# Kernel tuning notes

Hardware: AMD Instinct MI355X
Metric: run time of the kernel (lower is better)

## Reference

```python
import jax, jax.numpy as jnp
import numpy as np

B, C, H, W = 64, 256, 64, 64
HEADS = 8
Q = 16
FH = 512
EPS = 1e-6


def setup_inputs() -> dict:
    key = jax.random.key(0)
    ks = jax.random.split(key, 4)
    def init(k, shape, fan_in):
        return jax.random.normal(k, shape, jnp.float32) * (1.0 / np.sqrt(fan_in))
    return {
        "x": jax.random.normal(ks[0], (B, C, H, W), jnp.float32),
        "ln_gamma": jnp.ones((C,), jnp.float32),
        "ln_beta": jnp.zeros((C,), jnp.float32),
        # grouped 1x1 conv weight: torch shape [Q*h, C/h, 1, 1] -> [h, Q, C/h]
        "attn_w": init(ks[1], (HEADS, Q, C // HEADS), C // HEADS),
        "val_w": init(ks[2], (C, C), C),
        "val_b": jnp.zeros((C,), jnp.float32),
        "fin_w": init(ks[3], (FH, C * Q), C * Q),
        "fin_b": jnp.zeros((FH,), jnp.float32),
    }


def reference(x, ln_gamma, ln_beta, attn_w, val_w, val_b, fin_w, fin_b):
    B_, C_, H_, W_ = x.shape
    L = H_ * W_
    xf = x.reshape(B_, C_, L)  # [B, C, HW]
    # LayerNorm2d: normalize over channel dim (permute in torch == axis=1 here)
    mu = jnp.mean(xf, axis=1, keepdims=True)
    var = jnp.mean((xf - mu) ** 2, axis=1, keepdims=True)
    xn = (xf - mu) * jax.lax.rsqrt(var + EPS) * ln_gamma[:, None] + ln_beta[:, None]
    # grouped 1x1 conv: each head sees its own C/h channel slice
    xh = xn.reshape(B_, HEADS, C_ // HEADS, L)
    logits = jnp.einsum('hqc,bhcl->bhql', attn_w, xh)  # [B, h, Q, HW]
    Aw = jax.nn.softmax(logits, axis=-1)
    # value projection: full 1x1 conv with bias
    V = jnp.einsum('ec,bcl->bel', val_w, xn) + val_b[None, :, None]  # [B, C, HW]
    Vh = V.reshape(B_, HEADS, C_ // HEADS, L)
    # weighted pooling (bmm): [B, h, Q, d]
    A = jnp.einsum('bhql,bhdl->bhqd', Aw, Vh)
    Aflat = A.reshape(B_, Q * C_)  # matches torch reshape order (h, q, d)
    return Aflat @ fin_w.T + fin_b
```

## Files before the change

### kernel.cpp

```cpp
#include <hip/hip_runtime.h>

typedef unsigned short u16;
typedef unsigned int u32;

#define B_   64
#define C_   256
#define L_   4096
#define NH   8
#define NQ   16
#define DH   32
#define HQ   128
#define FHN  512
#define EPS_ 1e-6f

#define WS_WC    0
#define WS_SWG   8192
#define WS_CB    8704
#define WS_VGC   9216
#define WS_WG1   140288
#define WS_WB1   141312
#define WS_DENP  142336
#define WS_SNUP  404480
#define WS_A     666624
#define WS_APART 1715200

typedef __attribute__((ext_vector_type(8))) short bf16x8;
typedef __attribute__((ext_vector_type(4))) float f32x4;

__device__ __forceinline__ u16 f32_to_bf16(float f) {
    u32 u = __float_as_uint(f);
    u32 r = u + 0x7fffu + ((u >> 16) & 1u);
    return (u16)(r >> 16);
}
__device__ __forceinline__ float bf16_to_f32(u16 h) {
    return __uint_as_float(((u32)h) << 16);
}
__device__ __forceinline__ u32 pk2(u16 lo, u16 hi) {
    return (u32)lo | ((u32)hi << 16);
}

__global__ __launch_bounds__(256) void k_prep(
    const float* __restrict__ attn_w, const float* __restrict__ gamma,
    const float* __restrict__ beta, u16* __restrict__ wc,
    float* __restrict__ Swg, float* __restrict__ Cb)
{
    int t = threadIdx.x;
    if (t >= HQ) return;
    int h = t >> 4;
    float sw = 0.f, cb = 0.f;
    for (int c = 0; c < DH; c++) {
        float w = attn_w[t * DH + c];
        u16 hb = f32_to_bf16(w * gamma[h * DH + c]);
        wc[t * DH + c] = hb;
        sw += bf16_to_f32(hb);
        cb += w * beta[h * DH + c];
    }
    Swg[t] = sw;
    Cb[t] = cb;
}

__global__ __launch_bounds__(256) void k_prepv(
    const float* __restrict__ val_w, const float* __restrict__ gamma,
    const float* __restrict__ beta, u16* __restrict__ VGc,
    float* __restrict__ Wg1, float* __restrict__ Wb1)
{
    int t = threadIdx.x;
    int e = blockIdx.x * 4 + (t >> 6);
    int lane = t & 63;
    float4 w  = *(const float4*)(val_w + (size_t)e * C_ + lane * 4);
    float4 g  = *(const float4*)(gamma + lane * 4);
    float4 bt = *(const float4*)(beta + lane * 4);
    u16 h0 = f32_to_bf16(w.x * g.x);
    u16 h1 = f32_to_bf16(w.y * g.y);
    u16 h2 = f32_to_bf16(w.z * g.z);
    u16 h3 = f32_to_bf16(w.w * g.w);
    uint2 pk;
    pk.x = pk2(h0, h1);
    pk.y = pk2(h2, h3);
    *(uint2*)(VGc + (size_t)e * C_ + lane * 4) = pk;
    float sg = bf16_to_f32(h0) + bf16_to_f32(h1) + bf16_to_f32(h2) + bf16_to_f32(h3);
    float sb = w.x * bt.x + w.y * bt.y + w.z * bt.z + w.w * bt.w;
    #pragma unroll
    for (int off = 1; off < 64; off <<= 1) {
        sg += __shfl_xor(sg, off);
        sb += __shfl_xor(sb, off);
    }
    if (lane == 0) { Wg1[e] = sg; Wb1[e] = sb; }
}

__global__ __launch_bounds__(256) void k_fused(
    const float* __restrict__ x, const u16* __restrict__ wc,
    const float* __restrict__ Swg, const float* __restrict__ Cb,
    const u16* __restrict__ VGc, float* __restrict__ Apart,
    float* __restrict__ DenP, float* __restrict__ SnuP)
{
    __shared__ __align__(16) char POOL[67584];
    u16* const XT  = (u16*)POOL;
    u16* const EA  = (u16*)(POOL + 16896);
    u16* const XCb = (u16*)(POOL + 27136);
    __shared__ float smu[32], srs[32];
    int t = threadIdx.x;
    int lane = t & 63, wv = t >> 6;
    int lane15 = lane & 15, quad = lane >> 4;
    int ks = blockIdx.x, b = blockIdx.y;
    int lbase = ks * 512;
    int m0 = (wv & 1) * 64, n0 = (wv >> 1) * 128;

    bf16x8 af[2];
    float swr[2][4], cbr[2][4];
    #pragma unroll
    for (int s = 0; s < 2; s++) {
        int h = wv * 2 + s;
        af[s] = *(const bf16x8*)(wc + (size_t)(h * 16 + lane15) * DH + quad * 8);
        #pragma unroll
        for (int r = 0; r < 4; r++) {
            int hq = h * 16 + quad * 4 + r;
            swr[s][r] = Swg[hq];
            cbr[s][r] = Cb[hq];
        }
    }

    const float* xR = x + ((size_t)b * C_ + t) * L_ + lbase;

    float4 fr[8];
    uint4 pr[4];
    auto loadregs = [&](int k) {
        int o = k * 32;
        #pragma unroll
        for (int i = 0; i < 8; i++) fr[i] = *(const float4*)(xR + o + i * 4);
    };
    auto cvtregs = [&]() {
        const float* pf = (const float*)fr;
        u16 hh[32];
        #pragma unroll
        for (int e = 0; e < 32; e++) hh[e] = f32_to_bf16(pf[e]);
        #pragma unroll
        for (int i = 0; i < 4; i++) {
            uint4 w;
            w.x = pk2(hh[i * 8 + 0], hh[i * 8 + 1]);
            w.y = pk2(hh[i * 8 + 2], hh[i * 8 + 3]);
            w.z = pk2(hh[i * 8 + 4], hh[i * 8 + 5]);
            w.w = pk2(hh[i * 8 + 6], hh[i * 8 + 7]);
            pr[i] = w;
        }
    };
    auto write_xc = [&](int buf) {
        #pragma unroll
        for (int i = 0; i < 4; i++)
            *(uint4*)&XCb[buf * 8192 + t * 32 + ((i ^ (t & 3)) * 8)] = pr[i];
    };
    auto write_xt = [&]() {
        const u16* ph = (const u16*)pr;
        #pragma unroll
        for (int e = 0; e < 32; e++) XT[e * 264 + t] = ph[e];
    };

    f32x4 acc[4][8];
    #pragma unroll
    for (int i = 0; i < 4; i++)
        #pragma unroll
        for (int j = 0; j < 8; j++) {
            f32x4 z = {0.f, 0.f, 0.f, 0.f};
            acc[i][j] = z;
        }
    float se[2][4] = {}, sm[2][4] = {};

    int l_loc = t >> 3, g = t & 7;

    loadregs(0);
    cvtregs();
    write_xt();
    write_xc(0);
    loadregs(1);
    __syncthreads();

    for (int k = 0; k < 16; k++) {
        int cur = k & 1;

        {
            const u16* row = XT + l_loc * 264 + g * 32;
            float s = 0.f, q = 0.f;
            #pragma unroll
            for (int j = 0; j < 4; j++) {
                uint4 v = *(const uint4*)(row + j * 8);
                u32 ww[4] = {v.x, v.y, v.z, v.w};
                #pragma unroll
                for (int e = 0; e < 4; e++) {
                    float f0 = __uint_as_float(ww[e] << 16);
                    float f1 = __uint_as_float(ww[e] & 0xffff0000u);
                    s += f0 + f1;
                    q += f0 * f0 + f1 * f1;
                }
            }
            #pragma unroll
            for (int off = 1; off < 8; off <<= 1) {
                s += __shfl_xor(s, off);
                q += __shfl_xor(q, off);
            }
            if (g == 0) {
                float mm = s * (1.f / C_);
                float vv = fmaxf(q * (1.f / C_) - mm * mm, 0.f) + EPS_;
                smu[l_loc] = mm;
                srs[l_loc] = rsqrtf(vv);
            }
        }
        __syncthreads();

        #pragma unroll
        for (int half = 0; half < 2; half++) {
            float m_l = smu[half * 16 + lane15];
            float r_l = srs[half * 16 + lane15];
            #pragma unroll
            for (int s = 0; s < 2; s++) {
                int h = wv * 2 + s;
                bf16x8 bfrag = *(const bf16x8*)(XT + (half * 16 + lane15) * 264 + h * DH + quad * 8);
                f32x4 z = {0.f, 0.f, 0.f, 0.f};
                f32x4 c4 = __builtin_amdgcn_mfma_f32_16x16x32_bf16(af[s], bfrag, z, 0, 0, 0);
                #pragma unroll
                for (int r = 0; r < 4; r++) {
                    float logit = r_l * (c4[r] - m_l * swr[s][r]) + cbr[s][r];
                    float e = __expf(logit);
                    float ers = e * r_l;
                    EA[(h * 16 + quad * 4 + r) * 40 + half * 16 + lane15] = f32_to_bf16(ers);
                    se[s][r] += e;
                    sm[s][r] += ers * m_l;
                }
            }
        }
        __syncthreads();

        if (k < 15) { cvtregs(); write_xt(); write_xc(cur ^ 1); }
        if (k < 14) loadregs(k + 2);

        bf16x8 a[4];
        #pragma unroll
        for (int i = 0; i < 4; i++)
            a[i] = *(const bf16x8*)&EA[(m0 + i * 16 + lane15) * 40 + quad * 8];
        #pragma unroll
        for (int j = 0; j < 8; j++) {
            int row = n0 + j * 16 + lane15;
            bf16x8 bbj = *(const bf16x8*)&XCb[cur * 8192 + row * 32 + ((quad ^ (row & 3)) * 8)];
            #pragma unroll
            for (int i = 0; i < 4; i++)
                acc[i][j] = __builtin_amdgcn_mfma_f32_16x16x32_bf16(a[i], bbj, acc[i][j], 0, 0, 0);
        }
        __syncthreads();
    }

    u16* const P = (u16*)POOL;
    #pragma unroll
    for (int i = 0; i < 4; i++)
        #pragma unroll
        for (int j = 0; j < 8; j++) {
            int row = m0 + i * 16 + quad * 4;
            int col = n0 + j * 16 + lane15;
            #pragma unroll
            for (int r = 0; r < 4; r++)
                P[(row + r) * 264 + col] = f32_to_bf16(acc[i][j][r]);
        }
    __syncthreads();

    float* ApB = Apart + (((size_t)ks * B_ + b) * HQ) * DH;
    #pragma unroll
    for (int s = 0; s < 2; s++) {
        int h = wv * 2 + s;
        #pragma unroll
        for (int dt = 0; dt < 2; dt++) {
            f32x4 c2 = {0.f, 0.f, 0.f, 0.f};
            #pragma unroll
            for (int kk = 0; kk < 8; kk++) {
                bf16x8 a = *(const bf16x8*)&P[(h * 16 + lane15) * 264 + kk * 32 + quad * 8];
                bf16x8 vg = *(const bf16x8*)(VGc + (size_t)(h * DH + dt * 16 + lane15) * C_ + kk * 32 + quad * 8);
                c2 = __builtin_amdgcn_mfma_f32_16x16x32_bf16(a, vg, c2, 0, 0, 0);
            }
            #pragma unroll
            for (int r = 0; r < 4; r++)
                ApB[(size_t)(h * 16 + quad * 4 + r) * DH + dt * 16 + lane15] = c2[r];
        }
    }

    #pragma unroll
    for (int s = 0; s < 2; s++)
        #pragma unroll
        for (int r = 0; r < 4; r++) {
            float v = se[s][r], w = sm[s][r];
            #pragma unroll
            for (int off = 1; off < 16; off <<= 1) {
                v += __shfl_xor(v, off);
                w += __shfl_xor(w, off);
            }
            if (lane15 == 0) {
                int row = b * HQ + (wv * 2 + s) * 16 + quad * 4 + r;
                DenP[ks * (B_ * HQ) + row] = v;
                SnuP[ks * (B_ * HQ) + row] = w;
            }
        }
}

__global__ __launch_bounds__(256) void k_reduce(
    const float* __restrict__ Apart, const float* __restrict__ DenP,
    const float* __restrict__ SnuP, const float* __restrict__ Wg1,
    const float* __restrict__ Wb1, const float* __restrict__ val_b,
    float* __restrict__ A)
{
    __shared__ float sden[32], ssnu[32];
    int t = threadIdx.x;
    int q4 = blockIdx.x, b = blockIdx.y;
    int hq0 = q4 * 32;
    if (t < 32) {
        int row = b * HQ + hq0 + t;
        float d = 0.f, sn = 0.f;
        #pragma unroll
        for (int s = 0; s < 8; s++) {
            d  += DenP[s * (B_ * HQ) + row];
            sn += SnuP[s * (B_ * HQ) + row];
        }
        sden[t] = d;
        ssnu[t] = sn;
    }
    __syncthreads();
    #pragma unroll
    for (int i = 0; i < 4; i++) {
        int idx = i * 256 + t;
        int r32 = idx >> 5, d = idx & 31;
        int hq = hq0 + r32;
        float v = 0.f;
        #pragma unroll
        for (int s = 0; s < 8; s++)
            v += Apart[(((size_t)s * B_ + b) * HQ + hq) * DH + d];
        int hd = (hq >> 4) * DH + d;
        A[((size_t)b * HQ + hq) * DH + d] =
            (v - ssnu[r32] * Wg1[hd]) / sden[r32] + Wb1[hd] + val_b[hd];
    }
}

__global__ __launch_bounds__(256) void k_final(
    const float* __restrict__ A, const float* __restrict__ fin_w,
    const float* __restrict__ fin_b, float* __restrict__ out)
{
    __shared__ float At[64 * 129];
    __shared__ float Fw[32 * 129];
    int t = threadIdx.x;
    int kc = blockIdx.x, ft = blockIdx.y;
    int k0 = kc * 128;

    #pragma unroll
    for (int w = 0; w < 8; w++) {
        int s = t + w * 256;
        int row = s >> 5, seg = s & 31;
        float4 v = *(const float4*)(A + (size_t)row * 4096 + k0 + seg * 4);
        const float* pf = (const float*)&v;
        #pragma unroll
        for (int e = 0; e < 4; e++) At[row * 129 + seg * 4 + e] = pf[e];
    }
    #pragma unroll
    for (int w = 0; w < 4; w++) {
        int s = t + w * 256;
        int row = s >> 5, seg = s & 31;
        float4 v = *(const float4*)(fin_w + (size_t)(ft * 32 + row) * 4096 + k0 + seg * 4);
        const float* pf = (const float*)&v;
        #pragma unroll
        for (int e = 0; e < 4; e++) Fw[row * 129 + seg * 4 + e] = pf[e];
    }
    __syncthreads();

    int tb = t >> 3, tf = t & 7;
    float acc[2][4];
    #pragma unroll
    for (int e = 0; e < 2; e++)
        #pragma unroll
        for (int j = 0; j < 4; j++) acc[e][j] = 0.f;

    for (int k = 0; k < 128; k++) {
        float a0 = At[(tb * 2) * 129 + k];
        float a1 = At[(tb * 2 + 1) * 129 + k];
        #pragma unroll
        for (int j = 0; j < 4; j++) {
            float f = Fw[(tf * 4 + j) * 129 + k];
            acc[0][j] += a0 * f;
            acc[1][j] += a1 * f;
        }
    }
    #pragma unroll
    for (int e = 0; e < 2; e++) {
        int brow = tb * 2 + e;
        #pragma unroll
        for (int j = 0; j < 4; j++) {
            int f = ft * 32 + tf * 4 + j;
            float v = acc[e][j];
            if (kc == 0) v += fin_b[f];
            atomicAdd(&out[(size_t)brow * FHN + f], v);
        }
    }
}

extern "C" void kernel_launch(void* const* d_in, const int* in_sizes, int n_in,
                              void* d_out, int out_size, void* d_ws, size_t ws_size,
                              hipStream_t stream) {
    const float* x      = (const float*)d_in[0];
    const float* gamma  = (const float*)d_in[1];
    const float* beta   = (const float*)d_in[2];
    const float* attn_w = (const float*)d_in[3];
    const float* val_w  = (const float*)d_in[4];
    const float* val_b  = (const float*)d_in[5];
    const float* fin_w  = (const float*)d_in[6];
    const float* fin_b  = (const float*)d_in[7];
    float* out = (float*)d_out;
    char* ws = (char*)d_ws;

    u16*   wc    = (u16*)(ws + WS_WC);
    float* Swg   = (float*)(ws + WS_SWG);
    float* Cb    = (float*)(ws + WS_CB);
    u16*   VGc   = (u16*)(ws + WS_VGC);
    float* Wg1   = (float*)(ws + WS_WG1);
    float* Wb1   = (float*)(ws + WS_WB1);
    float* DenP  = (float*)(ws + WS_DENP);
    float* SnuP  = (float*)(ws + WS_SNUP);
    float* A     = (float*)(ws + WS_A);
    float* Apart = (float*)(ws + WS_APART);

    hipMemsetAsync(out, 0, (size_t)B_ * FHN * sizeof(float), stream);

    k_prep<<<dim3(1), dim3(256), 0, stream>>>(attn_w, gamma, beta, wc, Swg, Cb);
    k_prepv<<<dim3(64), dim3(256), 0, stream>>>(val_w, gamma, beta, VGc, Wg1, Wb1);
    k_fused<<<dim3(8, 64), dim3(256), 0, stream>>>(x, wc, Swg, Cb, VGc, Apart,
                                                   DenP, SnuP);
    k_reduce<<<dim3(4, 64), dim3(256), 0, stream>>>(Apart, DenP, SnuP, Wg1, Wb1,
                                                    val_b, A);
    k_final<<<dim3(32, 16), dim3(256), 0, stream>>>(A, fin_w, fin_b, out);
}
```

Measured before the change: 431.0 us.

## Double block to 512 threads, single-buffer XC, shrink per-wave tiles

Result: slower. 582.1 us (+35.1%).

```diff
diff --git a/kernel.cpp b/kernel.cpp
--- a/kernel.cpp
+++ b/kernel.cpp
@@ -88,100 +88,96 @@
     if (lane == 0) { Wg1[e] = sg; Wb1[e] = sb; }
 }
 
-__global__ __launch_bounds__(256) void k_fused(
+__global__ __launch_bounds__(512, 4) void k_fused(
     const float* __restrict__ x, const u16* __restrict__ wc,
     const float* __restrict__ Swg, const float* __restrict__ Cb,
     const u16* __restrict__ VGc, float* __restrict__ Apart,
     float* __restrict__ DenP, float* __restrict__ SnuP)
 {
-    __shared__ __align__(16) char POOL[67584];
-    u16* const XT  = (u16*)POOL;
-    u16* const EA  = (u16*)(POOL + 16896);
-    u16* const XCb = (u16*)(POOL + 27136);
+    __shared__ __align__(16) char POOL[42496];
+    u16* const XT = (u16*)POOL;
+    u16* const EA = (u16*)(POOL + 16896);
+    u16* const XC = (u16*)(POOL + 26112);
     __shared__ float smu[32], srs[32];
     int t = threadIdx.x;
     int lane = t & 63, wv = t >> 6;
     int lane15 = lane & 15, quad = lane >> 4;
     int ks = blockIdx.x, b = blockIdx.y;
     int lbase = ks * 512;
-    int m0 = (wv & 1) * 64, n0 = (wv >> 1) * 128;
-
-    bf16x8 af[2];
-    float swr[2][4], cbr[2][4];
-    #pragma unroll
-    for (int s = 0; s < 2; s++) {
-        int h = wv * 2 + s;
-        af[s] = *(const bf16x8*)(wc + (size_t)(h * 16 + lane15) * DH + quad * 8);
-        #pragma unroll
-        for (int r = 0; r < 4; r++) {
-            int hq = h * 16 + quad * 4 + r;
-            swr[s][r] = Swg[hq];
-            cbr[s][r] = Cb[hq];
-        }
-    }
-
-    const float* xR = x + ((size_t)b * C_ + t) * L_ + lbase;
-
-    float4 fr[8];
-    uint4 pr[4];
+    int m0 = (wv & 1) * 64, n0 = (wv >> 1) * 64;
+    int c_own = t & 255, hh = t >> 8;
+
+    int h = wv;
+    bf16x8 af = *(const bf16x8*)(wc + (size_t)(h * 16 + lane15) * DH + quad * 8);
+    float swr[4], cbr[4];
+    #pragma unroll
+    for (int r = 0; r < 4; r++) {
+        int hq = h * 16 + quad * 4 + r;
+        swr[r] = Swg[hq];
+        cbr[r] = Cb[hq];
+    }
+
+    const float* xR = x + ((size_t)b * C_ + c_own) * L_ + lbase + hh * 16;
+
+    float4 fr[4];
+    uint4 pr[2];
     auto loadregs = [&](int k) {
-        int o = k * 32;
-        #pragma unroll
-        for (int i = 0; i < 8; i++) fr[i] = *(const float4*)(xR + o + i * 4);
+        #pragma unroll
+        for (int i = 0; i < 4; i++) fr[i] = *(const float4*)(xR + k * 32 + i * 4);
     };
     auto cvtregs = [&]() {
         const float* pf = (const float*)fr;
-        u16 hh[32];
-        #pragma unroll
-        for (int e = 0; e < 32; e++) hh[e] = f32_to_bf16(pf[e]);
-        #pragma unroll
-        for (int i = 0; i < 4; i++) {
+        u16 hb[16];
+        #pragma unroll
+        for (int e = 0; e < 16; e++) hb[e] = f32_to_bf16(pf[e]);
+        #pragma unroll
+        for (int i = 0; i < 2; i++) {
             uint4 w;
-            w.x = pk2(hh[i * 8 + 0], hh[i * 8 + 1]);
-            w.y = pk2(hh[i * 8 + 2], hh[i * 8 + 3]);
-            w.z = pk2(hh[i * 8 + 4], hh[i * 8 + 5]);
-            w.w = pk2(hh[i * 8 + 6], hh[i * 8 + 7]);
+            w.x = pk2(hb[i * 8 + 0], hb[i * 8 + 1]);
+            w.y = pk2(hb[i * 8 + 2], hb[i * 8 + 3]);
+            w.z = pk2(hb[i * 8 + 4], hb[i * 8 + 5]);
+            w.w = pk2(hb[i * 8 + 6], hb[i * 8 + 7]);
             pr[i] = w;
         }
     };
-    auto write_xc = [&](int buf) {
-        #pragma unroll
-        for (int i = 0; i < 4; i++)
-            *(uint4*)&XCb[buf * 8192 + t * 32 + ((i ^ (t & 3)) * 8)] = pr[i];
+    auto write_xc = [&]() {
+        #pragma unroll
+        for (int i = 0; i < 2; i++) {
+            int g = hh * 2 + i;
+            *(uint4*)&XC[c_own * 32 + ((g ^ ((c_own >> 1) & 3)) * 8)] = pr[i];
+        }
     };
     auto write_xt = [&]() {
         const u16* ph = (const u16*)pr;
         #pragma unroll
-        for (int e = 0; e < 32; e++) XT[e * 264 + t] = ph[e];
+        for (int e = 0; e < 16; e++) XT[(hh * 16 + e) * 264 + c_own] = ph[e];
     };
 
-    f32x4 acc[4][8];
+    f32x4 acc[4][4];
     #pragma unroll
     for (int i = 0; i < 4; i++)
         #pragma unroll
-        for (int j = 0; j < 8; j++) {
+        for (int j = 0; j < 4; j++) {
             f32x4 z = {0.f, 0.f, 0.f, 0.f};
             acc[i][j] = z;
         }
-    float se[2][4] = {}, sm[2][4] = {};
-
-    int l_loc = t >> 3, g = t & 7;
+    float se[4] = {}, sm[4] = {};
+
+    int l_loc = t >> 4, g16 = t & 15;
 
     loadregs(0);
     cvtregs();
     write_xt();
-    write_xc(0);
     loadregs(1);
     __syncthreads();
 
     for (int k = 0; k < 16; k++) {
-        int cur = k & 1;
-
+        write_xc();
         {
-            const u16* row = XT + l_loc * 264 + g * 32;
+            const u16* row = XT + l_loc * 264 + g16 * 16;
             float s = 0.f, q = 0.f;
             #pragma unroll
-            for (int j = 0; j < 4; j++) {
+            for (int j = 0; j < 2; j++) {
                 uint4 v = *(const uint4*)(row + j * 8);
                 u32 ww[4] = {v.x, v.y, v.z, v.w};
                 #pragma unroll
@@ -193,11 +189,11 @@
                 }
             }
             #pragma unroll
-            for (int off = 1; off < 8; off <<= 1) {
+            for (int off = 1; off < 16; off <<= 1) {
                 s += __shfl_xor(s, off);
                 q += __shfl_xor(q, off);
             }
-            if (g == 0) {
+            if (g16 == 0) {
                 float mm = s * (1.f / C_);
                 float vv = fmaxf(q * (1.f / C_) - mm * mm, 0.f) + EPS_;
                 smu[l_loc] = mm;
@@ -210,91 +206,88 @@
         for (int half = 0; half < 2; half++) {
             float m_l = smu[half * 16 + lane15];
             float r_l = srs[half * 16 + lane15];
-            #pragma unroll
-            for (int s = 0; s < 2; s++) {
-                int h = wv * 2 + s;
-                bf16x8 bfrag = *(const bf16x8*)(XT + (half * 16 + lane15) * 264 + h * DH + quad * 8);
-                f32x4 z = {0.f, 0.f, 0.f, 0.f};
-                f32x4 c4 = __builtin_amdgcn_mfma_f32_16x16x32_bf16(af[s], bfrag, z, 0, 0, 0);
-                #pragma unroll
-                for (int r = 0; r < 4; r++) {
-                    float logit = r_l * (c4[r] - m_l * swr[s][r]) + cbr[s][r];
-                    float e = __expf(logit);
-                    float ers = e * r_l;
-                    EA[(h * 16 + quad * 4 + r) * 40 + half * 16 + lane15] = f32_to_bf16(ers);
-                    se[s][r] += e;
-                    sm[s][r] += ers * m_l;
-                }
+            bf16x8 bfrag = *(const bf16x8*)(XT + (half * 16 + lane15) * 264 + h * DH + quad * 8);
+            f32x4 z = {0.f, 0.f, 0.f, 0.f};
+            f32x4 c4 = __builtin_amdgcn_mfma_f32_16x16x32_bf16(af, bfrag, z, 0, 0, 0);
+            #pragma unroll
+            for (int r = 0; r < 4; r++) {
+                float logit = r_l * (c4[r] - m_l * swr[r]) + cbr[r];
+                float e = __expf(logit);
+                float ers = e * r_l;
+                EA[(h * 16 + quad * 4 + r) * 36 + half * 16 + lane15] = f32_to_bf16(ers);
+                se[r] += e;
+                sm[r] += ers * m_l;
             }
         }
+        if (k < 15) cvtregs();
+        if (k < 14) loadregs(k + 2);
         __syncthreads();
 
-        if (k < 15) { cvtregs(); write_xt(); write_xc(cur ^ 1); }
-        if (k < 14) loadregs(k + 2);
-
         bf16x8 a[4];
         #pragma unroll
         for (int i = 0; i < 4; i++)
-            a[i] = *(const bf16x8*)&EA[(m0 + i * 16 + lane15) * 40 + quad * 8];
-        #pragma unroll
-        for (int j = 0; j < 8; j++) {
+            a[i] = *(const bf16x8*)&EA[(m0 + i * 16 + lane15) * 36 + quad * 8];
+        #pragma unroll
+        for (int j = 0; j < 4; j++) {
             int row = n0 + j * 16 + lane15;
-            bf16x8 bbj = *(const bf16x8*)&XCb[cur * 8192 + row * 32 + ((quad ^ (row & 3)) * 8)];
+            bf16x8 bbj = *(const bf16x8*)&XC[row * 32 + ((quad ^ ((row >> 1) & 3)) * 8)];
             #pragma unroll
             for (int i = 0; i < 4; i++)
                 acc[i][j] = __builtin_amdgcn_mfma_f32_16x16x32_bf16(a[i], bbj, acc[i][j], 0, 0, 0);
         }
+        if (k < 15) write_xt();
         __syncthreads();
     }
 
     u16* const P = (u16*)POOL;
-    #pragma unroll
-    for (int i = 0; i < 4; i++)
-        #pragma unroll
-        for (int j = 0; j < 8; j++) {
-            int row = m0 + i * 16 + quad * 4;
-            int col = n0 + j * 16 + lane15;
-            #pragma unroll
-            for (int r = 0; r < 4; r++)
-                P[(row + r) * 264 + col] = f32_to_bf16(acc[i][j][r]);
-        }
-    __syncthreads();
-
     float* ApB = Apart + (((size_t)ks * B_ + b) * HQ) * DH;
     #pragma unroll
-    for (int s = 0; s < 2; s++) {
-        int h = wv * 2 + s;
-        #pragma unroll
-        for (int dt = 0; dt < 2; dt++) {
+    for (int half = 0; half < 2; half++) {
+        if ((wv & 1) == half) {
+            #pragma unroll
+            for (int i = 0; i < 4; i++)
+                #pragma unroll
+                for (int j = 0; j < 4; j++) {
+                    int lr = i * 16 + quad * 4;
+                    int col = n0 + j * 16 + lane15;
+                    #pragma unroll
+                    for (int r = 0; r < 4; r++)
+                        P[(lr + r) * 264 + col] = f32_to_bf16(acc[i][j][r]);
+                }
+        }
+        __syncthreads();
+        {
+            int hl = wv >> 1;
+            int he = half * 4 + hl;
+            int dt = wv & 1;
             f32x4 c2 = {0.f, 0.f, 0.f, 0.f};
             #pragma unroll
             for (int kk = 0; kk < 8; kk++) {
-                bf16x8 a = *(const bf16x8*)&P[(h * 16 + lane15) * 264 + kk * 32 + quad * 8];
-                bf16x8 vg = *(const bf16x8*)(VGc + (size_t)(h * DH + dt * 16 + lane15) * C_ + kk * 32 + quad * 8);
+                bf16x8 a = *(const bf16x8*)&P[(hl * 16 + lane15) * 264 + kk * 32 + quad * 8];
+                bf16x8 vg = *(const bf16x8*)(VGc + (size_t)(he * DH + dt * 16 + lane15) * C_ + kk * 32 + quad * 8);
                 c2 = __builtin_amdgcn_mfma_f32_16x16x32_bf16(a, vg, c2, 0, 0, 0);
             }
             #pragma unroll
             for (int r = 0; r < 4; r++)
-                ApB[(size_t)(h * 16 + quad * 4 + r) * DH + dt * 16 + lane15] = c2[r];
-        }
-    }
-
-    #pragma unroll
-    for (int s = 0; s < 2; s++)
-        #pragma unroll
-        for (int r = 0; r < 4; r++) {
-            float v = se[s][r], w = sm[s][r];
-            #pragma unroll
-            for (int off = 1; off < 16; off <<= 1) {
-                v += __shfl_xor(v, off);
-                w += __shfl_xor(w, off);
-            }
-            if (lane15 == 0) {
-                int row = b * HQ + (wv * 2 + s) * 16 + quad * 4 + r;
-                DenP[ks * (B_ * HQ) + row] = v;
-                SnuP[ks * (B_ * HQ) + row] = w;
-            }
-        }
+                ApB[(size_t)(he * 16 + quad * 4 + r) * DH + dt * 16 + lane15] = c2[r];
+        }
+        __syncthreads();
+    }
+
+    #pragma unroll
+    for (int r = 0; r < 4; r++) {
+        float v = se[r], w = sm[r];
+        #pragma unroll
+        for (int off = 1; off < 16; off <<= 1) {
+            v += __shfl_xor(v, off);
+            w += __shfl_xor(w, off);
+        }
+        if (lane15 == 0) {
+            int row = b * HQ + wv * 16 + quad * 4 + r;
+            DenP[ks * (B_ * HQ) + row] = v;
+            SnuP[ks * (B_ * HQ) + row] = w;
+        }
+    }
 }
 
 __global__ __launch_bounds__(256) void k_reduce(
@@ -423,7 +416,7 @@
 
     k_prep<<<dim3(1), dim3(256), 0, stream>>>(attn_w, gamma, beta, wc, Swg, Cb);
     k_prepv<<<dim3(64), dim3(256), 0, stream>>>(val_w, gamma, beta, VGc, Wg1, Wb1);
-    k_fused<<<dim3(8, 64), dim3(256), 0, stream>>>(x, wc, Swg, Cb, VGc, Apart,
+    k_fused<<<dim3(8, 64), dim3(512), 0, stream>>>(x, wc, Swg, Cb, VGc, Apart,
                                                    DenP, SnuP);
     k_reduce<<<dim3(4, 64), dim3(256), 0, stream>>>(Apart, DenP, SnuP, Wg1, Wb1,
                                                     val_b, A);
```

## Coalesce x loads across lanes and transpose via shuffles for XT writes

Applied to the files above, without the earlier changes.

Result: slower. 474.5 us (+10.1%).

```diff
diff --git a/kernel.cpp b/kernel.cpp
--- a/kernel.cpp
+++ b/kernel.cpp
@@ -88,7 +88,7 @@
     if (lane == 0) { Wg1[e] = sg; Wb1[e] = sb; }
 }
 
-__global__ __launch_bounds__(256) void k_fused(
+__global__ __launch_bounds__(256, 2) void k_fused(
     const float* __restrict__ x, const u16* __restrict__ wc,
     const float* __restrict__ Swg, const float* __restrict__ Cb,
     const u16* __restrict__ VGc, float* __restrict__ Apart,
@@ -106,6 +106,10 @@
     int lbase = ks * 512;
     int m0 = (wv & 1) * 64, n0 = (wv >> 1) * 128;
 
+    int lv = t & 7, rw = t >> 3;
+    int ti = rw & 3;
+    int cbase = rw & ~3;
+
     bf16x8 af[2];
     float swr[2][4], cbr[2][4];
     #pragma unroll
@@ -120,39 +124,57 @@
         }
     }
 
-    const float* xR = x + ((size_t)b * C_ + t) * L_ + lbase;
+    const float* xB = x + (size_t)b * C_ * L_ + lbase + lv * 4;
 
     float4 fr[8];
-    uint4 pr[4];
+    uint2 pr2[8];
     auto loadregs = [&](int k) {
-        int o = k * 32;
-        #pragma unroll
-        for (int i = 0; i < 8; i++) fr[i] = *(const float4*)(xR + o + i * 4);
+        #pragma unroll
+        for (int p = 0; p < 8; p++)
+            fr[p] = *(const float4*)(xB + (size_t)(p * 32 + rw) * L_ + k * 32);
     };
     auto cvtregs = [&]() {
-        const float* pf = (const float*)fr;
-        u16 hh[32];
-        #pragma unroll
-        for (int e = 0; e < 32; e++) hh[e] = f32_to_bf16(pf[e]);
-        #pragma unroll
-        for (int i = 0; i < 4; i++) {
-            uint4 w;
-            w.x = pk2(hh[i * 8 + 0], hh[i * 8 + 1]);
-            w.y = pk2(hh[i * 8 + 2], hh[i * 8 + 3]);
-            w.z = pk2(hh[i * 8 + 4], hh[i * 8 + 5]);
-            w.w = pk2(hh[i * 8 + 6], hh[i * 8 + 7]);
-            pr[i] = w;
+        #pragma unroll
+        for (int p = 0; p < 8; p++) {
+            pr2[p].x = pk2(f32_to_bf16(fr[p].x), f32_to_bf16(fr[p].y));
+            pr2[p].y = pk2(f32_to_bf16(fr[p].z), f32_to_bf16(fr[p].w));
         }
     };
     auto write_xc = [&](int buf) {
-        #pragma unroll
-        for (int i = 0; i < 4; i++)
-            *(uint4*)&XCb[buf * 8192 + t * 32 + ((i ^ (t & 3)) * 8)] = pr[i];
+        int g2 = lv >> 1, hl = (lv & 1) * 4;
+        #pragma unroll
+        for (int p = 0; p < 8; p++) {
+            int c = p * 32 + rw;
+            *(uint2*)&XCb[buf * 8192 + c * 32 + ((g2 ^ (c & 3)) * 8) + hl] = pr2[p];
+        }
+    };
+    auto transpose_pr = [&]() {
+        #pragma unroll
+        for (int p = 0; p < 8; p++) {
+            u32 a = pr2[p].x, bq = pr2[p].y;
+            u32 ta = __shfl_xor(a, 16);
+            u32 tb = __shfl_xor(bq, 16);
+            u32 A1 = (ti & 2) ? tb : a;
+            u32 B1 = (ti & 2) ? bq : ta;
+            u32 pA = __shfl_xor(A1, 8);
+            u32 pB = __shfl_xor(B1, 8);
+            u32 Af, Bf;
+            if ((ti & 1) == 0) {
+                Af = (A1 & 0xffffu) | (pA << 16);
+                Bf = (B1 & 0xffffu) | (pB << 16);
+            } else {
+                Af = (pA >> 16) | (A1 & 0xffff0000u);
+                Bf = (pB >> 16) | (B1 & 0xffff0000u);
+            }
+            pr2[p].x = Af;
+            pr2[p].y = Bf;
+        }
     };
     auto write_xt = [&]() {
-        const u16* ph = (const u16*)pr;
-        #pragma unroll
-        for (int e = 0; e < 32; e++) XT[e * 264 + t] = ph[e];
+        int l = 4 * lv + ti;
+        #pragma unroll
+        for (int p = 0; p < 8; p++)
+            *(uint2*)&XT[l * 264 + p * 32 + cbase] = pr2[p];
     };
 
     f32x4 acc[4][8];
@@ -169,8 +191,9 @@
 
     loadregs(0);
     cvtregs();
+    write_xc(0);
+    transpose_pr();
     write_xt();
-    write_xc(0);
     loadregs(1);
     __syncthreads();
 
@@ -229,7 +252,7 @@
         }
         __syncthreads();
 
-        if (k < 15) { cvtregs(); write_xt(); write_xc(cur ^ 1); }
+        if (k < 15) { cvtregs(); write_xc(cur ^ 1); transpose_pr(); write_xt(); }
         if (k < 14) loadregs(k + 2);
 
         bf16x8 a[4];
```
